# Optimization experiments

Measured on AMD Instinct MI355X. Metric: run time of the kernel, lower is better.

The kernel has to match this reference:

```python
import jax, jax.numpy as jnp
import numpy as np

T = 8          # number of adapter tasks
H = 1024       # hidden_size
I = 4096       # intermediate_size (bert dense input)
D = H // 16    # adapter bottleneck (reduction_factor=16)
B, S = 8, 512
EPS = 1e-12    # BERT LayerNorm eps


def _layernorm(x, g, b):
    mu = jnp.mean(x, axis=-1, keepdims=True)
    var = jnp.mean(jnp.square(x - mu), axis=-1, keepdims=True)
    return (x - mu) * jax.lax.rsqrt(var + EPS) * g + b


def setup_inputs() -> dict:
    key = jax.random.key(0)
    ks = jax.random.split(key, 14)
    std = 0.02
    inp = {
        "hidden_states": jax.random.normal(ks[0], (B, S, I), jnp.float32),
        "input_tensor": jax.random.normal(ks[1], (B, S, H), jnp.float32),
        "dense_w": jax.random.normal(ks[2], (H, I), jnp.float32) * std,
        "dense_b": jnp.zeros((H,), jnp.float32),
        "ln_g": jnp.ones((H,), jnp.float32),
        "ln_b": jnp.zeros((H,), jnp.float32),
        "down_w": jax.random.normal(ks[3], (T, D, H), jnp.float32) * std,
        "down_b": jnp.zeros((T, D), jnp.float32),
        "up_w": jax.random.normal(ks[4], (T, H, D), jnp.float32) * std,
        "up_b": jnp.zeros((T, H), jnp.float32),
        "key_w": jax.random.normal(ks[5], (H, H), jnp.float32) * std,
        "key_b": jnp.zeros((H,), jnp.float32),
        "query_w": jax.random.normal(ks[6], (H, H), jnp.float32) * std,
        "query_b": jnp.zeros((H,), jnp.float32),
        # value init: near-zero with identity diagonal
        "value_w": jnp.full((H, H), 1e-6, jnp.float32).at[jnp.arange(H), jnp.arange(H)].set(1.0),
    }
    return inp


def reference(hidden_states, input_tensor, dense_w, dense_b, ln_g, ln_b,
              down_w, down_b, up_w, up_b, key_w, key_b, query_w, query_b, value_w):
    # dense: [B,S,I] @ [H,I]^T -> [B,S,H]   (dropout = identity in eval)
    h = jnp.einsum('bsi,hi->bsh', hidden_states, dense_w) + dense_b
    prenorm = input_tensor + h
    adapter_in = _layernorm(prenorm, ln_g, ln_b)
    # batched per-task adapters: down-project, relu, up-project -> [T,B,S,H]
    down = jax.nn.relu(jnp.einsum('bsh,tdh->tbsd', adapter_in, down_w)
                       + down_b[:, None, None, :])
    adapter_out = jnp.einsum('tbsd,thd->tbsh', down, up_w) + up_b[:, None, None, :]
    # fusion attention over task axis T
    key = jnp.einsum('tbsh,kh->tbsk', adapter_out, key_w) + key_b
    value = jnp.einsum('tbsh,vh->tbsv', adapter_out + h[None], value_w)
    query = jnp.einsum('bsh,qh->bsq', prenorm, query_w) + query_b
    scores = jnp.sum(query[None] * key, axis=-1, keepdims=True)  # [T,B,S,1]
    probs = jax.nn.softmax(scores, axis=0)
    fusion = jnp.sum(probs * value, axis=0)                       # [B,S,H]
    return _layernorm(input_tensor + fusion, ln_g, ln_b)
```

## Files before the change

kernel.cpp:

```cpp
#include <hip/hip_runtime.h>
#include <cstdint>
#include <cstddef>

typedef float   f32x4 __attribute__((ext_vector_type(4)));
typedef _Float16 f16x8 __attribute__((ext_vector_type(8)));
typedef _Float16 f16x4 __attribute__((ext_vector_type(4)));

#define TOK  4096
#define HID  1024
#define IDIM 4096
#define LDP  40

#define GLDS16(gp, lp) __builtin_amdgcn_global_load_lds(                      \
    (const __attribute__((address_space(1))) void*)(gp),                      \
    (__attribute__((address_space(3))) void*)(lp), 16, 0, 0)

__global__ __launch_bounds__(256, 2) void gemm_dense(
    const _Float16* __restrict__ A, const _Float16* __restrict__ B,
    int K, int Kchunk, float* __restrict__ part)
{
    __shared__ _Float16 lA[128 * 32];
    __shared__ _Float16 lB[128 * 32];
    const int tid  = threadIdx.x;
    const int lane = tid & 63;
    const int wave = tid >> 6;
    const int m0   = blockIdx.x * 128;
    const int n0   = blockIdx.y * 128;
    const int kz0  = blockIdx.z * Kchunk;
    const int wM   = (wave & 1) * 64;
    const int wN   = (wave >> 1) * 64;

    const int srow = wave * 32 + (lane >> 2);
    const int scol = (lane & 3) * 8;
    const _Float16* gA = A + (size_t)(m0 + srow) * K + kz0 + scol;
    const _Float16* gB = B + (size_t)(n0 + srow) * K + kz0 + scol;
    _Float16* sA = lA + wave * 1024;
    _Float16* sB = lB + wave * 1024;

    f32x4 acc[4][4] = {};
    const int fr  = lane & 15;
    const int kc8 = (lane >> 4) * 8;

    for (int k = 0; k < Kchunk; k += 32) {
        GLDS16(gA + k,          sA);
        GLDS16(gA + k + 16 * K, sA + 512);
        GLDS16(gB + k,          sB);
        GLDS16(gB + k + 16 * K, sB + 512);
        __syncthreads();
        f16x8 afr[4], bfr[4];
#pragma unroll
        for (int mi = 0; mi < 4; ++mi)
            afr[mi] = *(const f16x8*)(lA + (wM + mi * 16 + fr) * 32 + kc8);
#pragma unroll
        for (int ni = 0; ni < 4; ++ni)
            bfr[ni] = *(const f16x8*)(lB + (wN + ni * 16 + fr) * 32 + kc8);
#pragma unroll
        for (int mi = 0; mi < 4; ++mi)
#pragma unroll
            for (int ni = 0; ni < 4; ++ni)
                acc[mi][ni] = __builtin_amdgcn_mfma_f32_16x16x32_f16(
                    afr[mi], bfr[ni], acc[mi][ni], 0, 0, 0);
        __syncthreads();
    }

    float* dst = part + (size_t)blockIdx.z * TOK * HID;
    const int cn = lane & 15;
    const int rq = (lane >> 4) * 4;
#pragma unroll
    for (int mi = 0; mi < 4; ++mi)
#pragma unroll
        for (int r = 0; r < 4; ++r) {
            const int m = m0 + wM + mi * 16 + rq + r;
#pragma unroll
            for (int ni = 0; ni < 4; ++ni) {
                const int n = n0 + wN + ni * 16 + cn;
                dst[(size_t)m * HID + n] = acc[mi][ni][r];
            }
        }
}

template <int MODE>
__global__ __launch_bounds__(1024, 4) void gemm_w32(
    const _Float16* __restrict__ Ah, const _Float16* __restrict__ B,
    int K, int Ncols,
    float* __restrict__ outF, _Float16* __restrict__ outH,
    const float* __restrict__ bias, const float* __restrict__ addv,
    const float* __restrict__ probs, const float* __restrict__ upb,
    const _Float16* __restrict__ A2, const _Float16* __restrict__ B2,
    _Float16* __restrict__ outH2)
{
    __shared__ _Float16 lA[128 * LDP];
    __shared__ _Float16 lB[128 * LDP];
    const int tid  = threadIdx.x;
    const int lane = tid & 63;
    const int wave = tid >> 6;
    const int m0   = blockIdx.x * 128;
    int n0, half = 0;
    const _Float16* Ap = Ah;
    const _Float16* Bp = B;
    if constexpr (MODE == 5) {
        half = blockIdx.y >> 2;
        n0 = (blockIdx.y & 3) * 128;
        if (half) { Ap = A2; Bp = B2; }
    } else {
        n0 = blockIdx.y * 128;
    }
    const int wM = (wave & 3) * 32;
    const int wN = (wave >> 2) * 32;

    f32x4 acc[2][2] = {};

    const int st   = tid & 511;
    const int srow = st >> 2;
    const int sc   = (st & 3) * 8;
    const _Float16* sbase = (tid < 512)
        ? Ap + (size_t)(m0 + srow) * K + sc
        : Bp + (size_t)(n0 + srow) * K + sc;
    _Float16* sdst = ((tid < 512) ? lA : lB) + srow * LDP + sc;

    for (int k0 = 0; k0 < K; k0 += 32) {
        *(uint4*)sdst = *(const uint4*)(sbase + k0);
        __syncthreads();
        const int fr  = lane & 15;
        const int kc8 = (lane >> 4) * 8;
        f16x8 afr[2], bfr[2];
#pragma unroll
        for (int mi = 0; mi < 2; ++mi)
            afr[mi] = *(const f16x8*)(lA + (wM + mi * 16 + fr) * LDP + kc8);
#pragma unroll
        for (int ni = 0; ni < 2; ++ni)
            bfr[ni] = *(const f16x8*)(lB + (wN + ni * 16 + fr) * LDP + kc8);
#pragma unroll
        for (int mi = 0; mi < 2; ++mi)
#pragma unroll
            for (int ni = 0; ni < 2; ++ni)
                acc[mi][ni] = __builtin_amdgcn_mfma_f32_16x16x32_f16(
                    afr[mi], bfr[ni], acc[mi][ni], 0, 0, 0);
        __syncthreads();
    }

    const int cn = lane & 15;
    const int rq = (lane >> 4) * 4;
#pragma unroll
    for (int mi = 0; mi < 2; ++mi)
#pragma unroll
        for (int r = 0; r < 4; ++r) {
            const int m = m0 + wM + mi * 16 + rq + r;
#pragma unroll
            for (int ni = 0; ni < 2; ++ni) {
                const int n = n0 + wN + ni * 16 + cn;
                const float v = acc[mi][ni][r];
                if constexpr (MODE == 1) {
                    const float bb = bias ? bias[n] : 0.f;
                    outH[(size_t)m * Ncols + n] = (_Float16)(v + bb);
                } else if constexpr (MODE == 3) {
                    const size_t idx = (size_t)m * Ncols + n;
                    float s = v + addv[idx];
#pragma unroll
                    for (int t = 0; t < 8; ++t)
                        s += probs[(size_t)m * 8 + t] * upb[t * 1024 + n];
                    outH[idx] = (_Float16)s;
                } else if constexpr (MODE == 4) {
                    const size_t idx = (size_t)m * Ncols + n;
                    outF[idx] = v + addv[idx];
                } else {
                    const size_t idx = (size_t)m * 512 + n;
                    if (half == 0) {
                        const float y = v + bias[n];
                        outH[idx] = (_Float16)(y > 0.f ? y : 0.f);
                    } else {
                        outH2[idx] = (_Float16)v;
                    }
                }
            }
        }
}

__global__ __launch_bounds__(256) void ln_fused(
    const float* __restrict__ part, int sk,
    const float* __restrict__ dbias, const float* __restrict__ it,
    const float* __restrict__ gam, const float* __restrict__ bet,
    float* __restrict__ h_f32, _Float16* __restrict__ ai, _Float16* __restrict__ pn)
{
    const int n = blockIdx.x, tid = threadIdx.x;
    const int lane = tid & 63, wave = tid >> 6;
    const size_t base = (size_t)n * 1024 + tid * 4;
    f32x4 h = *(const f32x4*)(dbias + tid * 4);
    for (int z = 0; z < sk; ++z)
        h += *(const f32x4*)(part + (size_t)z * TOK * HID + base);
    *(f32x4*)(h_f32 + base) = h;
    f32x4 x = h + *(const f32x4*)(it + base);
    float s = x[0] + x[1] + x[2] + x[3];
    float q = x[0] * x[0] + x[1] * x[1] + x[2] * x[2] + x[3] * x[3];
#pragma unroll
    for (int off = 1; off < 64; off <<= 1) {
        s += __shfl_xor(s, off);
        q += __shfl_xor(q, off);
    }
    __shared__ float rs[4], rq[4];
    if (lane == 0) { rs[wave] = s; rq[wave] = q; }
    __syncthreads();
    s = rs[0] + rs[1] + rs[2] + rs[3];
    q = rq[0] + rq[1] + rq[2] + rq[3];
    const float mu = s * (1.f / 1024.f);
    const float var = q * (1.f / 1024.f) - mu * mu;
    const float rstd = rsqrtf(var + 1e-12f);
    f32x4 gv = *(const f32x4*)(gam + tid * 4);
    f32x4 bv = *(const f32x4*)(bet + tid * 4);
    f16x4 av, pv;
#pragma unroll
    for (int j = 0; j < 4; ++j) {
        const float y = (x[j] - mu) * rstd * gv[j] + bv[j];
        av[j] = (_Float16)y;
        pv[j] = (_Float16)x[j];
    }
    *(f16x4*)(ai + base) = av;
    *(f16x4*)(pn + base) = pv;
}

__global__ __launch_bounds__(256) void ln_out(
    const float* __restrict__ fuse, const float* __restrict__ gam,
    const float* __restrict__ bet, float* __restrict__ outp)
{
    const int n = blockIdx.x, tid = threadIdx.x;
    const int lane = tid & 63, wave = tid >> 6;
    const size_t base = (size_t)n * 1024 + tid * 4;
    f32x4 x = *(const f32x4*)(fuse + base);
    float s = x[0] + x[1] + x[2] + x[3];
    float q = x[0] * x[0] + x[1] * x[1] + x[2] * x[2] + x[3] * x[3];
#pragma unroll
    for (int off = 1; off < 64; off <<= 1) {
        s += __shfl_xor(s, off);
        q += __shfl_xor(q, off);
    }
    __shared__ float rs[4], rq[4];
    if (lane == 0) { rs[wave] = s; rq[wave] = q; }
    __syncthreads();
    s = rs[0] + rs[1] + rs[2] + rs[3];
    q = rq[0] + rq[1] + rq[2] + rq[3];
    const float mu = s * (1.f / 1024.f);
    const float var = q * (1.f / 1024.f) - mu * mu;
    const float rstd = rsqrtf(var + 1e-12f);
    f32x4 gv = *(const f32x4*)(gam + tid * 4);
    f32x4 bv = *(const f32x4*)(bet + tid * 4);
    f32x4 y;
#pragma unroll
    for (int j = 0; j < 4; ++j) y[j] = (x[j] - mu) * rstd * gv[j] + bv[j];
    *(f32x4*)(outp + base) = y;
}

__global__ __launch_bounds__(256) void scores_softmax(
    const _Float16* __restrict__ qk, const _Float16* __restrict__ query,
    const float* __restrict__ key_b, const float* __restrict__ up_b,
    const _Float16* __restrict__ down, const _Float16* __restrict__ g,
    float* __restrict__ probs_out, _Float16* __restrict__ wdown)
{
    const int n = blockIdx.x, tid = threadIdx.x;
    const int lane = tid & 63, wave = tid >> 6;
    const _Float16* qkrow = qk + (size_t)n * 1024;
    const _Float16* qrow  = query + (size_t)n * 1024;
    float ub[8] = {};
    float qb = 0.f;
#pragma unroll
    for (int j = 0; j < 4; ++j) {
        const int h = tid + j * 256;
        const float qkv = (float)qkrow[h];
        qb += (float)qrow[h] * key_b[h];
#pragma unroll
        for (int t = 0; t < 8; ++t) ub[t] += qkv * up_b[t * 1024 + h];
    }
#pragma unroll
    for (int off = 1; off < 64; off <<= 1) {
        qb += __shfl_xor(qb, off);
#pragma unroll
        for (int t = 0; t < 8; ++t) ub[t] += __shfl_xor(ub[t], off);
    }
    __shared__ float red[4][9];
    __shared__ float sd[8];
    __shared__ float pl[8];
    if (lane == 0) {
        red[wave][0] = qb;
#pragma unroll
        for (int t = 0; t < 8; ++t) red[wave][1 + t] = ub[t];
    }
    const int c0 = tid * 2;
    const size_t dbase = (size_t)n * 512;
    const float d0 = (float)down[dbase + c0];
    const float d1 = (float)down[dbase + c0 + 1];
    float pz = d0 * (float)g[dbase + c0] + d1 * (float)g[dbase + c0 + 1];
#pragma unroll
    for (int off = 1; off < 32; off <<= 1) pz += __shfl_xor(pz, off);
    if ((lane & 31) == 0) sd[wave * 2 + (lane >> 5)] = pz;
    __syncthreads();
    if (tid == 0) {
        const float qbt = red[0][0] + red[1][0] + red[2][0] + red[3][0];
        float sc[8];
        float mx = -1e30f;
#pragma unroll
        for (int t = 0; t < 8; ++t) {
            sc[t] = sd[t] + qbt + red[0][1 + t] + red[1][1 + t] + red[2][1 + t] + red[3][1 + t];
            mx = fmaxf(mx, sc[t]);
        }
        float sum = 0.f;
#pragma unroll
        for (int t = 0; t < 8; ++t) { sc[t] = expf(sc[t] - mx); sum += sc[t]; }
        const float inv = 1.f / sum;
#pragma unroll
        for (int t = 0; t < 8; ++t) pl[t] = sc[t] * inv;
    }
    __syncthreads();
    const float pr = pl[c0 >> 6];
    wdown[dbase + c0]     = (_Float16)(pr * d0);
    wdown[dbase + c0 + 1] = (_Float16)(pr * d1);
    if (tid < 8) probs_out[(size_t)n * 8 + tid] = pl[tid];
}

__device__ inline void cvt_seg(const float* __restrict__ s, _Float16* __restrict__ d,
                               int n4, int gid, int gsz)
{
    for (int i = gid; i < n4; i += gsz) {
        f32x4 v = ((const f32x4*)s)[i];
        f16x4 o;
        o[0] = (_Float16)v[0]; o[1] = (_Float16)v[1];
        o[2] = (_Float16)v[2]; o[3] = (_Float16)v[3];
        ((f16x4*)d)[i] = o;
    }
}

__global__ __launch_bounds__(256) void convert5(
    const float* s0, _Float16* d0, int n0,
    const float* s1, _Float16* d1, int n1,
    const float* s2, _Float16* d2, int n2,
    const float* s3, _Float16* d3, int n3,
    const float* s4, _Float16* d4, int n4)
{
    const int gid = blockIdx.x * 256 + threadIdx.x;
    const int gsz = gridDim.x * 256;
    cvt_seg(s0, d0, n0, gid, gsz);
    cvt_seg(s1, d1, n1, gid, gsz);
    cvt_seg(s2, d2, n2, gid, gsz);
    cvt_seg(s3, d3, n3, gid, gsz);
    cvt_seg(s4, d4, n4, gid, gsz);
}

__global__ __launch_bounds__(256) void transpose_kw(
    const float* __restrict__ in, _Float16* __restrict__ outp)
{
    __shared__ float t[32][33];
    const int bx = blockIdx.x * 32;
    const int by = blockIdx.y * 32;
    const int tx = threadIdx.x & 31, ty = threadIdx.x >> 5;
#pragma unroll
    for (int j = 0; j < 32; j += 8)
        t[ty + j][tx] = in[(size_t)(by + ty + j) * 1024 + bx + tx];
    __syncthreads();
#pragma unroll
    for (int j = 0; j < 32; j += 8)
        outp[(size_t)(bx + ty + j) * 1024 + by + tx] = (_Float16)t[tx][ty + j];
}

__global__ __launch_bounds__(256) void reshape_up(
    const float* __restrict__ up_w, _Float16* __restrict__ upg,
    _Float16* __restrict__ upmix)
{
    const int i = blockIdx.x * 256 + threadIdx.x;
    const int d = i & 63;
    const int h = (i >> 6) & 1023;
    const int t = i >> 16;
    const float v = up_w[i];
    upg[(size_t)(t * 64 + d) * 1024 + h] = (_Float16)v;
    upmix[(size_t)h * 512 + t * 64 + d]  = (_Float16)v;
}

extern "C" void kernel_launch(void* const* d_in, const int* in_sizes, int n_in,
                              void* d_out, int out_size, void* d_ws, size_t ws_size,
                              hipStream_t stream)
{
    const float* hs      = (const float*)d_in[0];
    const float* it      = (const float*)d_in[1];
    const float* dense_w = (const float*)d_in[2];
    const float* dense_b = (const float*)d_in[3];
    const float* ln_g    = (const float*)d_in[4];
    const float* ln_b    = (const float*)d_in[5];
    const float* down_w  = (const float*)d_in[6];
    const float* down_b  = (const float*)d_in[7];
    const float* up_w    = (const float*)d_in[8];
    const float* up_b    = (const float*)d_in[9];
    const float* key_w   = (const float*)d_in[10];
    const float* key_b   = (const float*)d_in[11];
    const float* query_w = (const float*)d_in[12];
    const float* query_b = (const float*)d_in[13];
    const float* value_w = (const float*)d_in[14];
    float* outp = (float*)d_out;
    (void)in_sizes; (void)n_in; (void)out_size;

    const size_t MiB = 1ull << 20;
    char* p = (char*)d_ws;
    _Float16* w_dense = (_Float16*)p;  p += 8 * MiB;
    _Float16* w_query = (_Float16*)p;  p += 2 * MiB;
    _Float16* w_keyT  = (_Float16*)p;  p += 2 * MiB;
    _Float16* w_value = (_Float16*)p;  p += 2 * MiB;
    _Float16* w_down  = (_Float16*)p;  p += 1 * MiB;
    _Float16* w_upg   = (_Float16*)p;  p += 1 * MiB;
    _Float16* w_upmix = (_Float16*)p;  p += 1 * MiB;
    float*    h_f32   = (float*)p;     p += 16 * MiB;
    _Float16* ai      = (_Float16*)p;  p += 8 * MiB;
    _Float16* pn      = (_Float16*)p;  p += 8 * MiB;
    char* rb = p;
    const int sk = 2;
    float*    part  = (float*)rb;
    _Float16* hs_h  = (_Float16*)(rb + 32 * MiB);
    _Float16* query = (_Float16*)rb;
    _Float16* qk    = (_Float16*)(rb +  8 * MiB);
    _Float16* down  = (_Float16*)(rb + 16 * MiB);
    _Float16* g     = (_Float16*)(rb + 20 * MiB);
    _Float16* wdown = (_Float16*)(rb + 24 * MiB);
    float*    probs = (float*)(rb + 28 * MiB);
    float*    fuse  = (float*)rb;
    _Float16* mixed = ai;
    (void)ws_size;

    convert5<<<2048, 256, 0, stream>>>(hs, hs_h, TOK * IDIM / 4,
                                       dense_w, w_dense, HID * IDIM / 4,
                                       query_w, w_query, HID * HID / 4,
                                       value_w, w_value, HID * HID / 4,
                                       down_w,  w_down,  512 * HID / 4);
    transpose_kw<<<dim3(32, 32), 256, 0, stream>>>(key_w, w_keyT);
    reshape_up<<<2048, 256, 0, stream>>>(up_w, w_upg, w_upmix);

    gemm_dense<<<dim3(32, 8, sk), 256, 0, stream>>>(hs_h, w_dense, IDIM, IDIM / sk, part);
    ln_fused<<<TOK, 256, 0, stream>>>(part, sk, dense_b, it, ln_g, ln_b, h_f32, ai, pn);
    gemm_w32<1><<<dim3(32, 8), 1024, 0, stream>>>(
        pn, w_query, HID, HID, nullptr, query, query_b, nullptr, nullptr, nullptr,
        nullptr, nullptr, nullptr);
    gemm_w32<1><<<dim3(32, 8), 1024, 0, stream>>>(
        query, w_keyT, HID, HID, nullptr, qk, nullptr, nullptr, nullptr, nullptr,
        nullptr, nullptr, nullptr);
    gemm_w32<5><<<dim3(32, 8), 1024, 0, stream>>>(
        ai, w_down, HID, 512, nullptr, down, down_b, nullptr, nullptr, nullptr,
        qk, w_upg, g);
    scores_softmax<<<TOK, 256, 0, stream>>>(qk, query, key_b, up_b, down, g, probs, wdown);
    gemm_w32<3><<<dim3(32, 8), 1024, 0, stream>>>(
        wdown, w_upmix, 512, HID, nullptr, mixed, nullptr, h_f32, probs, up_b,
        nullptr, nullptr, nullptr);
    gemm_w32<4><<<dim3(32, 8), 1024, 0, stream>>>(
        mixed, w_value, HID, HID, fuse, nullptr, nullptr, it, nullptr, nullptr,
        nullptr, nullptr, nullptr);
    ln_out<<<TOK, 256, 0, stream>>>(fuse, ln_g, ln_b, outp);
}
```

Before: 384.6 us.

## Precompose query and key weights into one matrix and use k-major LDS tiles

Folds the query projection and the key projection into a single precomputed Wq^T·Wk weight, built from the weights alone. This drops one 4096x1024x1024 activation GEMM and the key_b term in scores, which is constant across tasks and cancels in softmax; the query bias is folded into a fused bias vector. The GEMM LDS tiles are relaid out k-major so global_load_lds can fill them directly in gemm_w32, replacing its register staging. Occupancy and split-K change, and hs_h is aliased onto h_f32.

```diff
diff --git a/kernel.cpp b/kernel.cpp
--- a/kernel.cpp
+++ b/kernel.cpp
@@ -9,18 +9,18 @@
 #define TOK  4096
 #define HID  1024
 #define IDIM 4096
-#define LDP  40
 
 #define GLDS16(gp, lp) __builtin_amdgcn_global_load_lds(                      \
     (const __attribute__((address_space(1))) void*)(gp),                      \
     (__attribute__((address_space(3))) void*)(lp), 16, 0, 0)
 
-__global__ __launch_bounds__(256, 2) void gemm_dense(
+
+__global__ __launch_bounds__(256, 4) void gemm_dense(
     const _Float16* __restrict__ A, const _Float16* __restrict__ B,
     int K, int Kchunk, float* __restrict__ part)
 {
-    __shared__ _Float16 lA[128 * 32];
-    __shared__ _Float16 lB[128 * 32];
+    __shared__ _Float16 lA[4096];
+    __shared__ _Float16 lB[4096];
     const int tid  = threadIdx.x;
     const int lane = tid & 63;
     const int wave = tid >> 6;
@@ -30,30 +30,30 @@
     const int wM   = (wave & 1) * 64;
     const int wN   = (wave >> 1) * 64;
 
-    const int srow = wave * 32 + (lane >> 2);
-    const int scol = (lane & 3) * 8;
-    const _Float16* gA = A + (size_t)(m0 + srow) * K + kz0 + scol;
-    const _Float16* gB = B + (size_t)(n0 + srow) * K + kz0 + scol;
-    _Float16* sA = lA + wave * 1024;
-    _Float16* sB = lB + wave * 1024;
+    const _Float16* gA0 = A + (size_t)(m0 + lane) * K + kz0 + wave * 8;
+    const _Float16* gA1 = gA0 + (size_t)64 * K;
+    const _Float16* gB0 = B + (size_t)(n0 + lane) * K + kz0 + wave * 8;
+    const _Float16* gB1 = gB0 + (size_t)64 * K;
+    _Float16* sA0 = lA + wave * 1024;
+    _Float16* sB0 = lB + wave * 1024;
 
     f32x4 acc[4][4] = {};
     const int fr  = lane & 15;
-    const int kc8 = (lane >> 4) * 8;
+    const int khr = lane >> 4;
 
     for (int k = 0; k < Kchunk; k += 32) {
-        GLDS16(gA + k,          sA);
-        GLDS16(gA + k + 16 * K, sA + 512);
-        GLDS16(gB + k,          sB);
-        GLDS16(gB + k + 16 * K, sB + 512);
+        GLDS16(gA0 + k, sA0);
+        GLDS16(gA1 + k, sA0 + 512);
+        GLDS16(gB0 + k, sB0);
+        GLDS16(gB1 + k, sB0 + 512);
         __syncthreads();
         f16x8 afr[4], bfr[4];
 #pragma unroll
         for (int mi = 0; mi < 4; ++mi)
-            afr[mi] = *(const f16x8*)(lA + (wM + mi * 16 + fr) * 32 + kc8);
+            afr[mi] = *(const f16x8*)(lA + (khr * 128 + wM + mi * 16 + fr) * 8);
 #pragma unroll
         for (int ni = 0; ni < 4; ++ni)
-            bfr[ni] = *(const f16x8*)(lB + (wN + ni * 16 + fr) * 32 + kc8);
+            bfr[ni] = *(const f16x8*)(lB + (khr * 128 + wN + ni * 16 + fr) * 8);
 #pragma unroll
         for (int mi = 0; mi < 4; ++mi)
 #pragma unroll
@@ -89,8 +89,8 @@
     const _Float16* __restrict__ A2, const _Float16* __restrict__ B2,
     _Float16* __restrict__ outH2)
 {
-    __shared__ _Float16 lA[128 * LDP];
-    __shared__ _Float16 lB[128 * LDP];
+    __shared__ _Float16 lA[4096];
+    __shared__ _Float16 lB[4096];
     const int tid  = threadIdx.x;
     const int lane = tid & 63;
     const int wave = tid >> 6;
@@ -110,26 +110,25 @@
 
     f32x4 acc[2][2] = {};
 
-    const int st   = tid & 511;
-    const int srow = st >> 2;
-    const int sc   = (st & 3) * 8;
-    const _Float16* sbase = (tid < 512)
-        ? Ap + (size_t)(m0 + srow) * K + sc
-        : Bp + (size_t)(n0 + srow) * K + sc;
-    _Float16* sdst = ((tid < 512) ? lA : lB) + srow * LDP + sc;
+    const int i8 = wave & 7;
+    const _Float16* gsrc = ((wave < 8)
+        ? Ap + (size_t)(m0 + (i8 & 1) * 64 + lane) * K
+        : Bp + (size_t)(n0 + (i8 & 1) * 64 + lane) * K) + (i8 >> 1) * 8;
+    _Float16* ldst = ((wave < 8) ? lA : lB) + i8 * 512;
+
+    const int fr  = lane & 15;
+    const int khr = lane >> 4;
 
     for (int k0 = 0; k0 < K; k0 += 32) {
-        *(uint4*)sdst = *(const uint4*)(sbase + k0);
+        GLDS16(gsrc + k0, ldst);
         __syncthreads();
-        const int fr  = lane & 15;
-        const int kc8 = (lane >> 4) * 8;
         f16x8 afr[2], bfr[2];
 #pragma unroll
         for (int mi = 0; mi < 2; ++mi)
-            afr[mi] = *(const f16x8*)(lA + (wM + mi * 16 + fr) * LDP + kc8);
+            afr[mi] = *(const f16x8*)(lA + (khr * 128 + wM + mi * 16 + fr) * 8);
 #pragma unroll
         for (int ni = 0; ni < 2; ++ni)
-            bfr[ni] = *(const f16x8*)(lB + (wN + ni * 16 + fr) * LDP + kc8);
+            bfr[ni] = *(const f16x8*)(lB + (khr * 128 + wN + ni * 16 + fr) * 8);
 #pragma unroll
         for (int mi = 0; mi < 2; ++mi)
 #pragma unroll
@@ -250,28 +249,23 @@
 }
 
 __global__ __launch_bounds__(256) void scores_softmax(
-    const _Float16* __restrict__ qk, const _Float16* __restrict__ query,
-    const float* __restrict__ key_b, const float* __restrict__ up_b,
+    const _Float16* __restrict__ qk, const float* __restrict__ up_b,
     const _Float16* __restrict__ down, const _Float16* __restrict__ g,
     float* __restrict__ probs_out, _Float16* __restrict__ wdown)
 {
     const int n = blockIdx.x, tid = threadIdx.x;
     const int lane = tid & 63, wave = tid >> 6;
     const _Float16* qkrow = qk + (size_t)n * 1024;
-    const _Float16* qrow  = query + (size_t)n * 1024;
     float ub[8] = {};
-    float qb = 0.f;
 #pragma unroll
     for (int j = 0; j < 4; ++j) {
         const int h = tid + j * 256;
         const float qkv = (float)qkrow[h];
-        qb += (float)qrow[h] * key_b[h];
 #pragma unroll
         for (int t = 0; t < 8; ++t) ub[t] += qkv * up_b[t * 1024 + h];
     }
 #pragma unroll
     for (int off = 1; off < 64; off <<= 1) {
-        qb += __shfl_xor(qb, off);
 #pragma unroll
         for (int t = 0; t < 8; ++t) ub[t] += __shfl_xor(ub[t], off);
     }
@@ -279,9 +273,8 @@
     __shared__ float sd[8];
     __shared__ float pl[8];
     if (lane == 0) {
-        red[wave][0] = qb;
-#pragma unroll
-        for (int t = 0; t < 8; ++t) red[wave][1 + t] = ub[t];
+#pragma unroll
+        for (int t = 0; t < 8; ++t) red[wave][t] = ub[t];
     }
     const int c0 = tid * 2;
     const size_t dbase = (size_t)n * 512;
@@ -293,12 +286,11 @@
     if ((lane & 31) == 0) sd[wave * 2 + (lane >> 5)] = pz;
     __syncthreads();
     if (tid == 0) {
-        const float qbt = red[0][0] + red[1][0] + red[2][0] + red[3][0];
         float sc[8];
         float mx = -1e30f;
 #pragma unroll
         for (int t = 0; t < 8; ++t) {
-            sc[t] = sd[t] + qbt + red[0][1 + t] + red[1][1 + t] + red[2][1 + t] + red[3][1 + t];
+            sc[t] = sd[t] + red[0][t] + red[1][t] + red[2][t] + red[3][t];
             mx = fmaxf(mx, sc[t]);
         }
         float sum = 0.f;
@@ -327,26 +319,31 @@
     }
 }
 
-__global__ __launch_bounds__(256) void convert5(
+__global__ __launch_bounds__(256) void convert4(
     const float* s0, _Float16* d0, int n0,
     const float* s1, _Float16* d1, int n1,
     const float* s2, _Float16* d2, int n2,
     const float* s3, _Float16* d3, int n3,
-    const float* s4, _Float16* d4, int n4)
-{
+    float* bz)
+{
+    if (blockIdx.x == 0) {
+        f32x4 z = {0.f, 0.f, 0.f, 0.f};
+        *(f32x4*)(bz + threadIdx.x * 4) = z;
+    }
     const int gid = blockIdx.x * 256 + threadIdx.x;
     const int gsz = gridDim.x * 256;
     cvt_seg(s0, d0, n0, gid, gsz);
     cvt_seg(s1, d1, n1, gid, gsz);
     cvt_seg(s2, d2, n2, gid, gsz);
     cvt_seg(s3, d3, n3, gid, gsz);
-    cvt_seg(s4, d4, n4, gid, gsz);
 }
 
 __global__ __launch_bounds__(256) void transpose_kw(
-    const float* __restrict__ in, _Float16* __restrict__ outp)
+    const float* __restrict__ in, _Float16* __restrict__ outp,
+    const float* __restrict__ rvec, float* __restrict__ rout)
 {
     __shared__ float t[32][33];
+    __shared__ float rpart[8][33];
     const int bx = blockIdx.x * 32;
     const int by = blockIdx.y * 32;
     const int tx = threadIdx.x & 31, ty = threadIdx.x >> 5;
@@ -357,6 +354,22 @@
 #pragma unroll
     for (int j = 0; j < 32; j += 8)
         outp[(size_t)(bx + ty + j) * 1024 + by + tx] = (_Float16)t[tx][ty + j];
+    if (rvec) {
+        float s = 0.f;
+#pragma unroll
+        for (int j = 0; j < 4; ++j) {
+            const int k = ty * 4 + j;
+            s += rvec[by + k] * t[k][tx];
+        }
+        rpart[ty][tx] = s;
+        __syncthreads();
+        if (ty == 0) {
+            float v = rpart[0][tx];
+#pragma unroll
+            for (int r = 1; r < 8; ++r) v += rpart[r][tx];
+            atomicAdd(rout + bx + tx, v);
+        }
+    }
 }
 
 __global__ __launch_bounds__(256) void reshape_up(
@@ -392,25 +405,26 @@
     const float* query_b = (const float*)d_in[13];
     const float* value_w = (const float*)d_in[14];
     float* outp = (float*)d_out;
-    (void)in_sizes; (void)n_in; (void)out_size;
+    (void)in_sizes; (void)n_in; (void)out_size; (void)key_b;
 
     const size_t MiB = 1ull << 20;
     char* p = (char*)d_ws;
-    _Float16* w_dense = (_Float16*)p;  p += 8 * MiB;
-    _Float16* w_query = (_Float16*)p;  p += 2 * MiB;
-    _Float16* w_keyT  = (_Float16*)p;  p += 2 * MiB;
-    _Float16* w_value = (_Float16*)p;  p += 2 * MiB;
-    _Float16* w_down  = (_Float16*)p;  p += 1 * MiB;
-    _Float16* w_upg   = (_Float16*)p;  p += 1 * MiB;
-    _Float16* w_upmix = (_Float16*)p;  p += 1 * MiB;
-    float*    h_f32   = (float*)p;     p += 16 * MiB;
-    _Float16* ai      = (_Float16*)p;  p += 8 * MiB;
-    _Float16* pn      = (_Float16*)p;  p += 8 * MiB;
+    _Float16* w_dense  = (_Float16*)p; p += 8 * MiB;
+    _Float16* w_queryT = (_Float16*)p; p += 2 * MiB;
+    _Float16* w_keyT   = (_Float16*)p; p += 2 * MiB;
+    _Float16* w_value  = (_Float16*)p; p += 2 * MiB;
+    _Float16* w_fuseT  = (_Float16*)p; p += 2 * MiB;
+    _Float16* w_down   = (_Float16*)p; p += 1 * MiB;
+    _Float16* w_upg    = (_Float16*)p; p += 1 * MiB;
+    _Float16* w_upmix  = (_Float16*)p; p += 1 * MiB;
+    float*    bfuse    = (float*)p;    p += 1 * MiB;
+    float*    h_f32    = (float*)p;    p += 16 * MiB;
+    _Float16* ai       = (_Float16*)p; p += 8 * MiB;
+    _Float16* pn       = (_Float16*)p; p += 8 * MiB;
+    _Float16* hs_h = (_Float16*)h_f32;
     char* rb = p;
-    const int sk = 2;
+    const int sk = (ws_size >= (size_t)(52 + 64) * MiB) ? 4 : 2;
     float*    part  = (float*)rb;
-    _Float16* hs_h  = (_Float16*)(rb + 32 * MiB);
-    _Float16* query = (_Float16*)rb;
     _Float16* qk    = (_Float16*)(rb +  8 * MiB);
     _Float16* down  = (_Float16*)(rb + 16 * MiB);
     _Float16* g     = (_Float16*)(rb + 20 * MiB);
@@ -418,28 +432,28 @@
     float*    probs = (float*)(rb + 28 * MiB);
     float*    fuse  = (float*)rb;
     _Float16* mixed = ai;
-    (void)ws_size;
-
-    convert5<<<2048, 256, 0, stream>>>(hs, hs_h, TOK * IDIM / 4,
+
+    convert4<<<2048, 256, 0, stream>>>(hs, hs_h, TOK * IDIM / 4,
                                        dense_w, w_dense, HID * IDIM / 4,
-                                       query_w, w_query, HID * HID / 4,
                                        value_w, w_value, HID * HID / 4,
-                                       down_w,  w_down,  512 * HID / 4);
-    transpose_kw<<<dim3(32, 32), 256, 0, stream>>>(key_w, w_keyT);
+                                       down_w,  w_down,  512 * HID / 4,
+                                       bfuse);
+    transpose_kw<<<dim3(32, 32), 256, 0, stream>>>(key_w, w_keyT, query_b, bfuse);
+    transpose_kw<<<dim3(32, 32), 256, 0, stream>>>(query_w, w_queryT, nullptr, nullptr);
     reshape_up<<<2048, 256, 0, stream>>>(up_w, w_upg, w_upmix);
+    gemm_w32<1><<<dim3(8, 8), 1024, 0, stream>>>(
+        w_keyT, w_queryT, HID, HID, nullptr, w_fuseT, nullptr, nullptr, nullptr,
+        nullptr, nullptr, nullptr, nullptr);
 
     gemm_dense<<<dim3(32, 8, sk), 256, 0, stream>>>(hs_h, w_dense, IDIM, IDIM / sk, part);
     ln_fused<<<TOK, 256, 0, stream>>>(part, sk, dense_b, it, ln_g, ln_b, h_f32, ai, pn);
     gemm_w32<1><<<dim3(32, 8), 1024, 0, stream>>>(
-        pn, w_query, HID, HID, nullptr, query, query_b, nullptr, nullptr, nullptr,
-        nullptr, nullptr, nullptr);
-    gemm_w32<1><<<dim3(32, 8), 1024, 0, stream>>>(
-        query, w_keyT, HID, HID, nullptr, qk, nullptr, nullptr, nullptr, nullptr,
+        pn, w_fuseT, HID, HID, nullptr, qk, bfuse, nullptr, nullptr, nullptr,
         nullptr, nullptr, nullptr);
     gemm_w32<5><<<dim3(32, 8), 1024, 0, stream>>>(
         ai, w_down, HID, 512, nullptr, down, down_b, nullptr, nullptr, nullptr,
         qk, w_upg, g);
-    scores_softmax<<<TOK, 256, 0, stream>>>(qk, query, key_b, up_b, down, g, probs, wdown);
+    scores_softmax<<<TOK, 256, 0, stream>>>(qk, up_b, down, g, probs, wdown);
     gemm_w32<3><<<dim3(32, 8), 1024, 0, stream>>>(
         wdown, w_upmix, 512, HID, nullptr, mixed, nullptr, h_f32, probs, up_b,
         nullptr, nullptr, nullptr);
```

Result: slower. 431.7 us (+12.2%).
